# Performance work log

Hardware: AMD Instinct MI355X
Metric: run time of the kernel (lower is better)

The kernel has to match this reference:

```python
import jax, jax.numpy as jnp
import numpy as np

B, L, D, H, DEPTH, K = 16, 2048, 256, 8, 2, 7
HD = D // H
SCALE = HD ** -0.5


def _ln(x, g, b, eps=1e-5):
    m = x.mean(-1, keepdims=True)
    v = ((x - m) ** 2).mean(-1, keepdims=True)
    return (x - m) * jax.lax.rsqrt(v + eps) * g + b


def _nat_attn(x, qkv_w, qkv_b, proj_w, proj_b):
    # Neighborhood attention 1D: window of K tokens centered on each token,
    # clamped at sequence edges (NATTEN semantics, dilation=1).
    b, l, d = x.shape
    qkv = (x @ qkv_w + qkv_b).reshape(b, l, 3, H, HD).transpose(2, 0, 3, 1, 4)  # [3,B,H,L,hd]
    q, k, v = qkv[0] * SCALE, qkv[1], qkv[2]
    starts = jnp.clip(jnp.arange(l) - K // 2, 0, l - K)          # [L]
    idx = starts[:, None] + jnp.arange(K)                        # [L,K]
    kn = k[:, :, idx]                                            # [B,H,L,K,hd]
    vn = v[:, :, idx]
    attn = jax.nn.softmax(jnp.einsum('bhld,bhlkd->bhlk', q, kn), axis=-1)
    out = jnp.einsum('bhlk,bhlkd->bhld', attn, vn)               # [B,H,L,hd]
    out = out.transpose(0, 2, 1, 3).reshape(b, l, d)
    return out @ proj_w + proj_b


def _mlp(x, w1, b1, w2, b2):
    return jax.nn.gelu(x @ w1 + b1, approximate=False) @ w2 + b2


def setup_inputs() -> dict:
    key = jax.random.key(0)
    ks = jax.random.split(key, 8)
    s = 0.02
    return {
        'x': jax.random.normal(ks[0], (B, L, D), jnp.float32),
        'ln1_g': jnp.ones((DEPTH, D), jnp.float32),
        'ln1_b': jnp.zeros((DEPTH, D), jnp.float32),
        'qkv_w': jax.random.normal(ks[1], (DEPTH, D, 3 * D), jnp.float32) * s,
        'qkv_b': jnp.zeros((DEPTH, 3 * D), jnp.float32),
        'proj_w': jax.random.normal(ks[2], (DEPTH, D, D), jnp.float32) * s,
        'proj_b': jnp.zeros((DEPTH, D), jnp.float32),
        'ln2_g': jnp.ones((DEPTH, D), jnp.float32),
        'ln2_b': jnp.zeros((DEPTH, D), jnp.float32),
        'fc1_w': jax.random.normal(ks[3], (DEPTH, D, 4 * D), jnp.float32) * s,
        'fc1_b': jnp.zeros((DEPTH, 4 * D), jnp.float32),
        'fc2_w': jax.random.normal(ks[4], (DEPTH, 4 * D, D), jnp.float32) * s,
        'fc2_b': jnp.zeros((DEPTH, D), jnp.float32),
        'conv_w': jax.random.normal(ks[5], (2 * D, D, 3), jnp.float32) * s,  # OIH
        'dn_g': jnp.ones((2 * D,), jnp.float32),
        'dn_b': jnp.zeros((2 * D,), jnp.float32),
    }


def reference(x, ln1_g, ln1_b, qkv_w, qkv_b, proj_w, proj_b,
              ln2_g, ln2_b, fc1_w, fc1_b, fc2_w, fc2_b,
              conv_w, dn_g, dn_b):
    for i in range(DEPTH):
        h = _nat_attn(_ln(x, ln1_g[i], ln1_b[i]), qkv_w[i], qkv_b[i], proj_w[i], proj_b[i])
        x = x + h
        x = x + _mlp(_ln(x, ln2_g[i], ln2_b[i]), fc1_w[i], fc1_b[i], fc2_w[i], fc2_b[i])
    # ConvDownsampler: Conv1d(D, 2D, k=3, s=2, p=1, bias=False) + LayerNorm
    xc = x.transpose(0, 2, 1)  # [B,C,L]
    y = jax.lax.conv_general_dilated(xc, conv_w, window_strides=(2,),
                                     padding=[(1, 1)],
                                     dimension_numbers=('NCH', 'OIH', 'NCH'))
    y = y.transpose(0, 2, 1)   # [B, L//2, 2D]
    y = _ln(y, dn_g, dn_b)
    return (y, x)
```

## Files before the change

### kernel.cpp

```cpp
#include <hip/hip_runtime.h>

typedef unsigned short u16;
typedef __attribute__((ext_vector_type(8))) short bf16x8;
typedef __attribute__((ext_vector_type(4))) float f32x4;

__device__ __forceinline__ float bf2f(u16 u) { return __uint_as_float(((unsigned)u) << 16); }
__device__ __forceinline__ u16 f2bf(float f) {
    unsigned u = __float_as_uint(f);
    return (u16)((u + 0x7FFFu + ((u >> 16) & 1u)) >> 16);
}

__device__ __forceinline__ float gelu_fast(float v) {
    float u = v * (1.5957691216057308f + 0.07135481282700722f * v * v);
    return v * (1.f / (1.f + __expf(-u)));
}

__device__ __forceinline__ void load_lds16(const u16* g, u16* l) {
    __builtin_amdgcn_global_load_lds(
        (const __attribute__((address_space(1))) unsigned int*)g,
        (__attribute__((address_space(3))) unsigned int*)l,
        16, 0, 0);
}

template<int EPI>
__global__ __launch_bounds__(256) void gemm_kernel(
    const u16* __restrict__ A, const u16* __restrict__ Wt,
    const float* __restrict__ bias, const float* __restrict__ res,
    void* __restrict__ outp, int M, int N, int K)
{
    __shared__ __align__(16) u16 As[128 * 32];
    __shared__ __align__(16) u16 Bs[128 * 32];
    const int tid  = threadIdx.x;
    const int lane = tid & 63;
    const int wave = tid >> 6;
    const int row0 = blockIdx.x * 128;
    const int col0 = blockIdx.y * 128;
    const int wr = (wave >> 1) * 64;
    const int wc = (wave & 1) * 64;
    const int lr = lane & 15;
    const int kq = (lane >> 4) * 8;

    f32x4 acc[4][4];
#pragma unroll
    for (int i = 0; i < 4; ++i)
#pragma unroll
        for (int j = 0; j < 4; ++j) acc[i][j] = (f32x4){0.f, 0.f, 0.f, 0.f};

    const int srow = tid >> 2;
    const int scol = (tid & 3) * 8;
    const u16* ag = A  + (size_t)(row0 + srow) * K + scol;
    const u16* bg = Wt + (size_t)(col0 + srow) * K + scol;
    const size_t rstep = (size_t)64 * K;
    u16* alp = As + tid * 8;
    u16* blp = Bs + tid * 8;

    for (int k0 = 0; k0 < K; k0 += 32) {
        __syncthreads();
        load_lds16(ag + k0,         alp);
        load_lds16(ag + rstep + k0, alp + 64 * 32);
        load_lds16(bg + k0,         blp);
        load_lds16(bg + rstep + k0, blp + 64 * 32);
        __syncthreads();
        bf16x8 af[4], bfv[4];
#pragma unroll
        for (int i = 0; i < 4; ++i) af[i]  = *(const bf16x8*)(As + (wr + i * 16 + lr) * 32 + kq);
#pragma unroll
        for (int j = 0; j < 4; ++j) bfv[j] = *(const bf16x8*)(Bs + (wc + j * 16 + lr) * 32 + kq);
#pragma unroll
        for (int i = 0; i < 4; ++i)
#pragma unroll
            for (int j = 0; j < 4; ++j)
                acc[i][j] = __builtin_amdgcn_mfma_f32_16x16x32_bf16(af[i], bfv[j], acc[i][j], 0, 0, 0);
    }

#pragma unroll
    for (int i = 0; i < 4; ++i) {
        const int rbase = row0 + wr + i * 16 + (lane >> 4) * 4;
#pragma unroll
        for (int j = 0; j < 4; ++j) {
            const int col = col0 + wc + j * 16 + lr;
            const float bv = (EPI == 3) ? 0.f : bias[col];
#pragma unroll
            for (int r = 0; r < 4; ++r) {
                const int row = rbase + r;
                float v = acc[i][j][r] + bv;
                if (EPI == 1) {
                    v += res[(size_t)row * N + col];
                    ((float*)outp)[(size_t)row * N + col] = v;
                } else {
                    if (EPI == 2) v = gelu_fast(v);
                    ((u16*)outp)[(size_t)row * N + col] = f2bf(v);
                }
            }
        }
    }
}

__global__ __launch_bounds__(256) void ln_f2b_kernel(
    const float* __restrict__ x, const float* __restrict__ g,
    const float* __restrict__ be, u16* __restrict__ out)
{
    const int lane = threadIdx.x & 63;
    const int row  = blockIdx.x * 4 + (threadIdx.x >> 6);
    const float4 a = *(const float4*)(x + (size_t)row * 256 + lane * 4);
    float v[4] = {a.x, a.y, a.z, a.w};
    float s = v[0] + v[1] + v[2] + v[3];
#pragma unroll
    for (int m = 1; m < 64; m <<= 1) s += __shfl_xor(s, m);
    const float mean = s * (1.f / 256.f);
    float s2 = 0.f;
#pragma unroll
    for (int e = 0; e < 4; ++e) { float d = v[e] - mean; s2 += d * d; }
#pragma unroll
    for (int m = 1; m < 64; m <<= 1) s2 += __shfl_xor(s2, m);
    const float rstd = rsqrtf(s2 * (1.f / 256.f) + 1e-5f);
    const float4 gg = *(const float4*)(g + lane * 4);
    const float4 bb = *(const float4*)(be + lane * 4);
    ushort4 o;
    o.x = f2bf((v[0] - mean) * rstd * gg.x + bb.x);
    o.y = f2bf((v[1] - mean) * rstd * gg.y + bb.y);
    o.z = f2bf((v[2] - mean) * rstd * gg.z + bb.z);
    o.w = f2bf((v[3] - mean) * rstd * gg.w + bb.w);
    *(ushort4*)(out + (size_t)row * 256 + lane * 4) = o;
}

__global__ __launch_bounds__(256) void ln_b2f_kernel(
    const u16* __restrict__ x, const float* __restrict__ g,
    const float* __restrict__ be, float* __restrict__ out)
{
    const int lane = threadIdx.x & 63;
    const int row  = blockIdx.x * 4 + (threadIdx.x >> 6);
    const u16* xr = x + (size_t)row * 512 + lane * 8;
    float v[8];
#pragma unroll
    for (int e = 0; e < 8; e += 4) {
        ushort4 a = *(const ushort4*)(xr + e);
        v[e] = bf2f(a.x); v[e+1] = bf2f(a.y); v[e+2] = bf2f(a.z); v[e+3] = bf2f(a.w);
    }
    float s = 0.f;
#pragma unroll
    for (int e = 0; e < 8; ++e) s += v[e];
#pragma unroll
    for (int m = 1; m < 64; m <<= 1) s += __shfl_xor(s, m);
    const float mean = s * (1.f / 512.f);
    float s2 = 0.f;
#pragma unroll
    for (int e = 0; e < 8; ++e) { float d = v[e] - mean; s2 += d * d; }
#pragma unroll
    for (int m = 1; m < 64; m <<= 1) s2 += __shfl_xor(s2, m);
    const float rstd = rsqrtf(s2 * (1.f / 512.f) + 1e-5f);
    float* orow = out + (size_t)row * 512 + lane * 8;
#pragma unroll
    for (int e = 0; e < 8; e += 4) {
        float4 o;
        o.x = (v[e]   - mean) * rstd * g[lane*8+e]   + be[lane*8+e];
        o.y = (v[e+1] - mean) * rstd * g[lane*8+e+1] + be[lane*8+e+1];
        o.z = (v[e+2] - mean) * rstd * g[lane*8+e+2] + be[lane*8+e+2];
        o.w = (v[e+3] - mean) * rstd * g[lane*8+e+3] + be[lane*8+e+3];
        *(float4*)(orow + e) = o;
    }
}

__global__ __launch_bounds__(256) void attn_kernel(
    const u16* __restrict__ qkv, u16* __restrict__ out)
{
    const int lane  = threadIdx.x & 63;
    const int token = blockIdx.x * 4 + (threadIdx.x >> 6);
    const int b = token >> 11;
    const int l = token & 2047;
    const int h = lane >> 3;
    const int s = lane & 7;
    const int off = h * 32 + s * 4;

    ushort4 q4 = *(const ushort4*)(qkv + (size_t)token * 768 + off);
    const float scale = 0.17677669529663687f;
    float q0 = bf2f(q4.x), q1 = bf2f(q4.y), q2 = bf2f(q4.z), q3 = bf2f(q4.w);

    int start = l - 3;
    start = start < 0 ? 0 : (start > 2041 ? 2041 : start);
    const u16* kbase = qkv + ((size_t)(b << 11) + start) * 768 + 256 + off;

    float sc[7], vv[7][4];
#pragma unroll
    for (int j = 0; j < 7; ++j) {
        const u16* kp = kbase + (size_t)j * 768;
        ushort4 k4 = *(const ushort4*)kp;
        ushort4 v4 = *(const ushort4*)(kp + 256);
        float d = q0 * bf2f(k4.x) + q1 * bf2f(k4.y) + q2 * bf2f(k4.z) + q3 * bf2f(k4.w);
        d += __shfl_xor(d, 1); d += __shfl_xor(d, 2); d += __shfl_xor(d, 4);
        sc[j] = d * scale;
        vv[j][0] = bf2f(v4.x); vv[j][1] = bf2f(v4.y); vv[j][2] = bf2f(v4.z); vv[j][3] = bf2f(v4.w);
    }
    float mx = sc[0];
#pragma unroll
    for (int j = 1; j < 7; ++j) mx = fmaxf(mx, sc[j]);
    float p[7], sum = 0.f;
#pragma unroll
    for (int j = 0; j < 7; ++j) { p[j] = expf(sc[j] - mx); sum += p[j]; }
    const float inv = 1.f / sum;
    float o0 = 0, o1 = 0, o2 = 0, o3 = 0;
#pragma unroll
    for (int j = 0; j < 7; ++j) {
        o0 += p[j] * vv[j][0]; o1 += p[j] * vv[j][1];
        o2 += p[j] * vv[j][2]; o3 += p[j] * vv[j][3];
    }
    ushort4 o;
    o.x = f2bf(o0 * inv); o.y = f2bf(o1 * inv); o.z = f2bf(o2 * inv); o.w = f2bf(o3 * inv);
    *(ushort4*)(out + (size_t)token * 256 + off) = o;
}

__global__ void transpose_kernel(const float* __restrict__ in, u16* __restrict__ out,
                                 int K, int N, int total)
{
    int idx = blockIdx.x * 256 + threadIdx.x;
    if (idx >= total) return;
    int k = idx % K;
    int n = (idx / K) % N;
    int d = idx / (K * N);
    out[idx] = f2bf(in[(size_t)d * K * N + (size_t)k * N + n]);
}

__global__ void convw_kernel(const float* __restrict__ in, u16* __restrict__ out)
{
    int idx = blockIdx.x * 256 + threadIdx.x;
    int r  = idx % 768;
    int co = idx / 768;
    int t  = r / 256;
    int ci = r % 256;
    out[idx] = f2bf(in[(size_t)co * 768 + (size_t)ci * 3 + t]);
}

__global__ __launch_bounds__(256) void im2col_kernel(
    const float* __restrict__ x, u16* __restrict__ x2, int r0)
{
    int idx = blockIdx.x * 256 + threadIdx.x;
    int c4  = idx & 63;
    int t   = (idx >> 6) % 3;
    int rl  = idx / 192;
    int row = r0 + rl;
    int b   = row >> 10;
    int lo  = row & 1023;
    int l   = 2 * lo + t - 1;
    ushort4 o = {0, 0, 0, 0};
    if (l >= 0 && l < 2048) {
        float4 val = *(const float4*)(x + ((size_t)(b << 11) + l) * 256 + c4 * 4);
        o.x = f2bf(val.x); o.y = f2bf(val.y); o.z = f2bf(val.z); o.w = f2bf(val.w);
    }
    *(ushort4*)(x2 + (size_t)rl * 768 + t * 256 + c4 * 4) = o;
}

extern "C" void kernel_launch(void* const* d_in, const int* in_sizes, int n_in,
                              void* d_out, int out_size, void* d_ws, size_t ws_size,
                              hipStream_t stream)
{
    const float* x_in   = (const float*)d_in[0];
    const float* ln1_g  = (const float*)d_in[1];
    const float* ln1_b  = (const float*)d_in[2];
    const float* qkv_w  = (const float*)d_in[3];
    const float* qkv_b  = (const float*)d_in[4];
    const float* proj_w = (const float*)d_in[5];
    const float* proj_b = (const float*)d_in[6];
    const float* ln2_g  = (const float*)d_in[7];
    const float* ln2_b  = (const float*)d_in[8];
    const float* fc1_w  = (const float*)d_in[9];
    const float* fc1_b  = (const float*)d_in[10];
    const float* fc2_w  = (const float*)d_in[11];
    const float* fc2_b  = (const float*)d_in[12];
    const float* conv_w = (const float*)d_in[13];
    const float* dn_g   = (const float*)d_in[14];
    const float* dn_b   = (const float*)d_in[15];

    float* xbuf = (float*)d_out + 8388608;
    u16*   xn   = (u16*)d_out;

    char* ws = (char*)d_ws;
    const size_t MB = 1024ull * 1024;
    u16* qkv_wt  = (u16*)ws;
    u16* proj_wt = qkv_wt  + 2 * 768 * 256;
    u16* fc1_wt  = proj_wt + 2 * 256 * 256;
    u16* fc2_wt  = fc1_wt  + 2 * 1024 * 256;
    u16* conv_wt = fc2_wt  + 2 * 256 * 1024;
    u16* S       = (u16*)(ws + 4 * MB);

    const size_t R = ws_size > 4 * MB ? ws_size - 4 * MB : 0;
    int nb = 16;    while (nb > 1 && (size_t)nb * 4 * MB > R) nb >>= 1;
    int Mf = 32768; while (Mf > 2048 && (size_t)Mf * 2048 > R) Mf >>= 1;
    int Mc = 16384; while (Mc > 2048 && (size_t)Mc * 2560 > R) Mc >>= 1;

    transpose_kernel<<<(2*256*768 + 255) / 256, 256, 0, stream>>>(qkv_w,  qkv_wt,  256, 768, 2*256*768);
    transpose_kernel<<<(2*256*256 + 255) / 256, 256, 0, stream>>>(proj_w, proj_wt, 256, 256, 2*256*256);
    transpose_kernel<<<(2*256*1024 + 255) / 256, 256, 0, stream>>>(fc1_w, fc1_wt,  256, 1024, 2*256*1024);
    transpose_kernel<<<(2*1024*256 + 255) / 256, 256, 0, stream>>>(fc2_w, fc2_wt,  1024, 256, 2*1024*256);
    convw_kernel<<<(512*768) / 256, 256, 0, stream>>>(conv_w, conv_wt);

    hipMemcpyAsync(xbuf, x_in, 32768ull * 256 * 4, hipMemcpyDeviceToDevice, stream);

    for (int layer = 0; layer < 2; ++layer) {
        const float* l1g = ln1_g + layer * 256;
        const float* l1b = ln1_b + layer * 256;
        const float* l2g = ln2_g + layer * 256;
        const float* l2b = ln2_b + layer * 256;
        const u16*   qwt = qkv_wt  + (size_t)layer * 768 * 256;
        const float* qb  = qkv_b   + layer * 768;
        const u16*   pwt = proj_wt + (size_t)layer * 256 * 256;
        const float* pb  = proj_b  + layer * 256;
        const u16*   f1w = fc1_wt  + (size_t)layer * 1024 * 256;
        const float* f1b = fc1_b   + layer * 1024;
        const u16*   f2w = fc2_wt  + (size_t)layer * 256 * 1024;
        const float* f2b = fc2_b   + layer * 256;

        ln_f2b_kernel<<<8192, 256, 0, stream>>>(xbuf, l1g, l1b, xn);
        {
            const int Mg = nb * 2048;
            u16* qkvc  = S;
            u16* atnoc = S + (size_t)Mg * 768;
            for (int g = 0; g < 16 / nb; ++g) {
                const size_t t0 = (size_t)g * Mg;
                gemm_kernel<0><<<dim3(Mg / 128, 6), 256, 0, stream>>>(
                    xn + t0 * 256, qwt, qb, nullptr, qkvc, Mg, 768, 256);
                attn_kernel<<<Mg / 4, 256, 0, stream>>>(qkvc, atnoc);
                gemm_kernel<1><<<dim3(Mg / 128, 2), 256, 0, stream>>>(
                    atnoc, pwt, pb, xbuf + t0 * 256, xbuf + t0 * 256, Mg, 256, 256);
            }
        }
        ln_f2b_kernel<<<8192, 256, 0, stream>>>(xbuf, l2g, l2b, xn);
        {
            u16* hbuf = S;
            for (int q = 0; q < 32768 / Mf; ++q) {
                const size_t r0 = (size_t)q * Mf;
                gemm_kernel<2><<<dim3(Mf / 128, 8), 256, 0, stream>>>(
                    xn + r0 * 256, f1w, f1b, nullptr, hbuf, Mf, 1024, 256);
                gemm_kernel<1><<<dim3(Mf / 128, 2), 256, 0, stream>>>(
                    hbuf, f2w, f2b, xbuf + r0 * 256, xbuf + r0 * 256, Mf, 256, 1024);
            }
        }
    }

    {
        u16* x2c = S;
        u16* ycc = S + (size_t)Mc * 768;
        for (int c = 0; c < 16384 / Mc; ++c) {
            const int r0 = c * Mc;
            im2col_kernel<<<3 * Mc / 4, 256, 0, stream>>>(xbuf, x2c, r0);
            gemm_kernel<3><<<dim3(Mc / 128, 4), 256, 0, stream>>>(
                x2c, conv_wt, nullptr, nullptr, ycc, Mc, 512, 768);
            ln_b2f_kernel<<<Mc / 4, 256, 0, stream>>>(
                ycc, dn_g, dn_b, (float*)d_out + (size_t)r0 * 512);
        }
    }
}
```

Before: 525.4 us.

## Add K=256 GEMM kernel with LDS-resident weight panel and register-prefetched A

Adds a GEMM variant for K=256 that loads a full 128-column weight panel (pre-swizzled on device into an 8-wide K-chunk layout) into LDS once per block. Each block then walks several 128-row tiles, reading A fragments straight from global memory into registers with a three-deep prefetch instead of staging A in LDS with barriers. It is used for the QKV, proj and fc1 GEMMs, and the weights for those are repacked by a new swizzle kernel. The 64KB LDS per block limits occupancy, and the old gemm_kernel's GELU branch was removed (it now serves only fc2 and conv, which don't need GELU).

```diff
diff --git a/kernel.cpp b/kernel.cpp
--- a/kernel.cpp
+++ b/kernel.cpp
@@ -20,6 +20,89 @@
         (const __attribute__((address_space(1))) unsigned int*)g,
         (__attribute__((address_space(3))) unsigned int*)l,
         16, 0, 0);
+}
+
+template<int RT, int EPI>
+__global__ __launch_bounds__(256, 2) void gemm3_kernel(
+    const u16* __restrict__ A, const u16* __restrict__ Wsw,
+    const float* __restrict__ bias, const float* __restrict__ res,
+    void* __restrict__ outp, int M, int N)
+{
+    __shared__ __align__(16) u16 Bs[128 * 256];
+    const int tid  = threadIdx.x;
+    const int lane = tid & 63;
+    const int wave = tid >> 6;
+    const int pan  = blockIdx.y;
+    const int rowS = blockIdx.x * (RT * 128);
+    const int wr = (wave >> 1) * 64;
+    const int wc = (wave & 1) * 64;
+    const int lr = lane & 15;
+    const int kq = lane >> 4;
+
+    const u16* wsrc = Wsw + (size_t)pan * (256 * 128);
+#pragma unroll
+    for (int p = 0; p < 16; ++p)
+        load_lds16(wsrc + p * 2048 + tid * 8, Bs + p * 2048 + tid * 8);
+    __syncthreads();
+
+    const int col00 = pan * 128;
+    for (int rt = 0; rt < RT; ++rt) {
+        const int row0 = rowS + rt * 128;
+        const u16* arow = A + (size_t)(row0 + wr + lr) * 256 + kq * 8;
+
+        f32x4 acc[4][4];
+#pragma unroll
+        for (int i = 0; i < 4; ++i)
+#pragma unroll
+            for (int j = 0; j < 4; ++j) acc[i][j] = (f32x4){0.f, 0.f, 0.f, 0.f};
+
+        bf16x8 af[3][4];
+#pragma unroll
+        for (int i = 0; i < 4; ++i) af[0][i] = *(const bf16x8*)(arow + (size_t)i * 16 * 256);
+#pragma unroll
+        for (int i = 0; i < 4; ++i) af[1][i] = *(const bf16x8*)(arow + (size_t)i * 16 * 256 + 32);
+
+#pragma unroll
+        for (int kk = 0; kk < 8; ++kk) {
+            if (kk + 2 < 8) {
+                const int ko = (kk + 2) * 32;
+#pragma unroll
+                for (int i = 0; i < 4; ++i)
+                    af[(kk + 2) % 3][i] = *(const bf16x8*)(arow + (size_t)i * 16 * 256 + ko);
+            }
+            bf16x8 bfv[4];
+#pragma unroll
+            for (int j = 0; j < 4; ++j)
+                bfv[j] = *(const bf16x8*)(Bs + (size_t)((kk * 4 + kq) * 128 + wc + j * 16 + lr) * 8);
+#pragma unroll
+            for (int i = 0; i < 4; ++i)
+#pragma unroll
+                for (int j = 0; j < 4; ++j)
+                    acc[i][j] = __builtin_amdgcn_mfma_f32_16x16x32_bf16(af[kk % 3][i], bfv[j], acc[i][j], 0, 0, 0);
+        }
+
+#pragma unroll
+        for (int i = 0; i < 4; ++i) {
+            const int rbase = row0 + wr + i * 16 + (lane >> 4) * 4;
+#pragma unroll
+            for (int j = 0; j < 4; ++j) {
+                const int col = col00 + wc + j * 16 + lr;
+                const float bv = bias[col];
+#pragma unroll
+                for (int r = 0; r < 4; ++r) {
+                    const int row = rbase + r;
+                    float v = acc[i][j][r] + bv;
+                    if (EPI == 1) {
+                        v += res[(size_t)row * N + col];
+                        ((float*)outp)[(size_t)row * N + col] = v;
+                    } else {
+                        if (EPI == 2) v = gelu_fast(v);
+                        ((u16*)outp)[(size_t)row * N + col] = f2bf(v);
+                    }
+                }
+            }
+        }
+    }
 }
 
 template<int EPI>
@@ -88,12 +171,52 @@
                     v += res[(size_t)row * N + col];
                     ((float*)outp)[(size_t)row * N + col] = v;
                 } else {
-                    if (EPI == 2) v = gelu_fast(v);
                     ((u16*)outp)[(size_t)row * N + col] = f2bf(v);
                 }
             }
         }
     }
+}
+
+__global__ void wswz_kernel(const float* __restrict__ in, u16* __restrict__ out,
+                            int K, int N, int total)
+{
+    int g = blockIdx.x * 256 + threadIdx.x;
+    if (g >= total) return;
+    int nl  = g & 127;
+    int t   = g >> 7;
+    int kqq = t % (K >> 3);
+    int dp  = t / (K >> 3);
+    int p   = dp % (N >> 7);
+    int d   = dp / (N >> 7);
+    int n_g = p * 128 + nl;
+    int k0  = kqq * 8;
+    const float* s = in + ((size_t)d * K + k0) * N + n_g;
+    u16 o[8];
+#pragma unroll
+    for (int e = 0; e < 8; ++e) o[e] = f2bf(s[(size_t)e * N]);
+    *(uint4*)(out + (size_t)g * 8) = *(const uint4*)o;
+}
+
+__global__ void transpose_kernel(const float* __restrict__ in, u16* __restrict__ out,
+                                 int K, int N, int total)
+{
+    int idx = blockIdx.x * 256 + threadIdx.x;
+    if (idx >= total) return;
+    int k = idx % K;
+    int n = (idx / K) % N;
+    int d = idx / (K * N);
+    out[idx] = f2bf(in[(size_t)d * K * N + (size_t)k * N + n]);
+}
+
+__global__ void convw_kernel(const float* __restrict__ in, u16* __restrict__ out)
+{
+    int idx = blockIdx.x * 256 + threadIdx.x;
+    int r  = idx % 768;
+    int co = idx / 768;
+    int t  = r / 256;
+    int ci = r % 256;
+    out[idx] = f2bf(in[(size_t)co * 768 + (size_t)ci * 3 + t]);
 }
 
 __global__ __launch_bounds__(256) void ln_f2b_kernel(
@@ -207,27 +330,6 @@
     ushort4 o;
     o.x = f2bf(o0 * inv); o.y = f2bf(o1 * inv); o.z = f2bf(o2 * inv); o.w = f2bf(o3 * inv);
     *(ushort4*)(out + (size_t)token * 256 + off) = o;
-}
-
-__global__ void transpose_kernel(const float* __restrict__ in, u16* __restrict__ out,
-                                 int K, int N, int total)
-{
-    int idx = blockIdx.x * 256 + threadIdx.x;
-    if (idx >= total) return;
-    int k = idx % K;
-    int n = (idx / K) % N;
-    int d = idx / (K * N);
-    out[idx] = f2bf(in[(size_t)d * K * N + (size_t)k * N + n]);
-}
-
-__global__ void convw_kernel(const float* __restrict__ in, u16* __restrict__ out)
-{
-    int idx = blockIdx.x * 256 + threadIdx.x;
-    int r  = idx % 768;
-    int co = idx / 768;
-    int t  = r / 256;
-    int ci = r % 256;
-    out[idx] = f2bf(in[(size_t)co * 768 + (size_t)ci * 3 + t]);
 }
 
 __global__ __launch_bounds__(256) void im2col_kernel(
@@ -287,10 +389,10 @@
     int Mf = 32768; while (Mf > 2048 && (size_t)Mf * 2048 > R) Mf >>= 1;
     int Mc = 16384; while (Mc > 2048 && (size_t)Mc * 2560 > R) Mc >>= 1;
 
-    transpose_kernel<<<(2*256*768 + 255) / 256, 256, 0, stream>>>(qkv_w,  qkv_wt,  256, 768, 2*256*768);
-    transpose_kernel<<<(2*256*256 + 255) / 256, 256, 0, stream>>>(proj_w, proj_wt, 256, 256, 2*256*256);
-    transpose_kernel<<<(2*256*1024 + 255) / 256, 256, 0, stream>>>(fc1_w, fc1_wt,  256, 1024, 2*256*1024);
-    transpose_kernel<<<(2*1024*256 + 255) / 256, 256, 0, stream>>>(fc2_w, fc2_wt,  1024, 256, 2*1024*256);
+    wswz_kernel<<<(2*256*768/8 + 255) / 256, 256, 0, stream>>>(qkv_w,  qkv_wt,  256, 768,  2*256*768/8);
+    wswz_kernel<<<(2*256*256/8 + 255) / 256, 256, 0, stream>>>(proj_w, proj_wt, 256, 256,  2*256*256/8);
+    wswz_kernel<<<(2*256*1024/8 + 255) / 256, 256, 0, stream>>>(fc1_w, fc1_wt,  256, 1024, 2*256*1024/8);
+    transpose_kernel<<<(2*1024*256 + 255) / 256, 256, 0, stream>>>(fc2_w, fc2_wt, 1024, 256, 2*1024*256);
     convw_kernel<<<(512*768) / 256, 256, 0, stream>>>(conv_w, conv_wt);
 
     hipMemcpyAsync(xbuf, x_in, 32768ull * 256 * 4, hipMemcpyDeviceToDevice, stream);
@@ -316,11 +418,11 @@
             u16* atnoc = S + (size_t)Mg * 768;
             for (int g = 0; g < 16 / nb; ++g) {
                 const size_t t0 = (size_t)g * Mg;
-                gemm_kernel<0><<<dim3(Mg / 128, 6), 256, 0, stream>>>(
-                    xn + t0 * 256, qwt, qb, nullptr, qkvc, Mg, 768, 256);
+                gemm3_kernel<4, 0><<<dim3(Mg / 512, 6), 256, 0, stream>>>(
+                    xn + t0 * 256, qwt, qb, nullptr, qkvc, Mg, 768);
                 attn_kernel<<<Mg / 4, 256, 0, stream>>>(qkvc, atnoc);
-                gemm_kernel<1><<<dim3(Mg / 128, 2), 256, 0, stream>>>(
-                    atnoc, pwt, pb, xbuf + t0 * 256, xbuf + t0 * 256, Mg, 256, 256);
+                gemm3_kernel<2, 1><<<dim3(Mg / 256, 2), 256, 0, stream>>>(
+                    atnoc, pwt, pb, xbuf + t0 * 256, xbuf + t0 * 256, Mg, 256);
             }
         }
         ln_f2b_kernel<<<8192, 256, 0, stream>>>(xbuf, l2g, l2b, xn);
@@ -328,8 +430,8 @@
             u16* hbuf = S;
             for (int q = 0; q < 32768 / Mf; ++q) {
                 const size_t r0 = (size_t)q * Mf;
-                gemm_kernel<2><<<dim3(Mf / 128, 8), 256, 0, stream>>>(
-                    xn + r0 * 256, f1w, f1b, nullptr, hbuf, Mf, 1024, 256);
+                gemm3_kernel<4, 2><<<dim3(Mf / 512, 8), 256, 0, stream>>>(
+                    xn + r0 * 256, f1w, f1b, nullptr, hbuf, Mf, 1024);
                 gemm_kernel<1><<<dim3(Mf / 128, 2), 256, 0, stream>>>(
                     hbuf, f2w, f2b, xbuf + r0 * 256, xbuf + r0 * 256, Mf, 256, 1024);
             }
```

Result: slower. 545.3 us (+3.8%).

## Double GEMM K-tile to 64 and XOR-swizzle LDS layout to avoid bank conflicts

Applied to the files above, without the earlier changes.

The GEMM main loop now stages a 128x64 K-slice per iteration instead of 128x32, which halves the number of barrier pairs per K. Each thread's global-to-LDS chunk index is XOR-swizzled by its row, and fragment reads apply the same swizzle so LDS reads hit fewer bank conflicts. LDS use per block doubles to 32 KB, which may reduce occupancy, and K must be a multiple of 64.

```diff
diff --git a/kernel.cpp b/kernel.cpp
--- a/kernel.cpp
+++ b/kernel.cpp
@@ -28,8 +28,8 @@
     const float* __restrict__ bias, const float* __restrict__ res,
     void* __restrict__ outp, int M, int N, int K)
 {
-    __shared__ __align__(16) u16 As[128 * 32];
-    __shared__ __align__(16) u16 Bs[128 * 32];
+    __shared__ __align__(16) u16 As[128 * 64];
+    __shared__ __align__(16) u16 Bs[128 * 64];
     const int tid  = threadIdx.x;
     const int lane = tid & 63;
     const int wave = tid >> 6;
@@ -38,7 +38,7 @@
     const int wr = (wave >> 1) * 64;
     const int wc = (wave & 1) * 64;
     const int lr = lane & 15;
-    const int kq = (lane >> 4) * 8;
+    const int q  = lane >> 4;
 
     f32x4 acc[4][4];
 #pragma unroll
@@ -46,31 +46,41 @@
 #pragma unroll
         for (int j = 0; j < 4; ++j) acc[i][j] = (f32x4){0.f, 0.f, 0.f, 0.f};
 
-    const int srow = tid >> 2;
-    const int scol = (tid & 3) * 8;
-    const u16* ag = A  + (size_t)(row0 + srow) * K + scol;
-    const u16* bg = Wt + (size_t)(col0 + srow) * K + scol;
-    const size_t rstep = (size_t)64 * K;
+    const int strow  = tid >> 3;
+    const int schunk = (tid & 7) ^ (strow & 7);
+    const u16* ag = A  + (size_t)(row0 + strow) * K + schunk * 8;
+    const u16* bg = Wt + (size_t)(col0 + strow) * K + schunk * 8;
+    const size_t rstep32 = (size_t)32 * K;
     u16* alp = As + tid * 8;
     u16* blp = Bs + tid * 8;
 
-    for (int k0 = 0; k0 < K; k0 += 32) {
+    for (int k0 = 0; k0 < K; k0 += 64) {
         __syncthreads();
-        load_lds16(ag + k0,         alp);
-        load_lds16(ag + rstep + k0, alp + 64 * 32);
-        load_lds16(bg + k0,         blp);
-        load_lds16(bg + rstep + k0, blp + 64 * 32);
+#pragma unroll
+        for (int s = 0; s < 4; ++s) {
+            load_lds16(ag + s * rstep32 + k0, alp + s * 2048);
+            load_lds16(bg + s * rstep32 + k0, blp + s * 2048);
+        }
         __syncthreads();
-        bf16x8 af[4], bfv[4];
-#pragma unroll
-        for (int i = 0; i < 4; ++i) af[i]  = *(const bf16x8*)(As + (wr + i * 16 + lr) * 32 + kq);
-#pragma unroll
-        for (int j = 0; j < 4; ++j) bfv[j] = *(const bf16x8*)(Bs + (wc + j * 16 + lr) * 32 + kq);
-#pragma unroll
-        for (int i = 0; i < 4; ++i)
-#pragma unroll
-            for (int j = 0; j < 4; ++j)
-                acc[i][j] = __builtin_amdgcn_mfma_f32_16x16x32_bf16(af[i], bfv[j], acc[i][j], 0, 0, 0);
+#pragma unroll
+        for (int kk = 0; kk < 2; ++kk) {
+            bf16x8 af[4], bfv[4];
+#pragma unroll
+            for (int i = 0; i < 4; ++i) {
+                const int r = wr + i * 16 + lr;
+                af[i] = *(const bf16x8*)(As + r * 64 + (((kk * 4 + q) ^ (r & 7)) * 8));
+            }
+#pragma unroll
+            for (int j = 0; j < 4; ++j) {
+                const int r = wc + j * 16 + lr;
+                bfv[j] = *(const bf16x8*)(Bs + r * 64 + (((kk * 4 + q) ^ (r & 7)) * 8));
+            }
+#pragma unroll
+            for (int i = 0; i < 4; ++i)
+#pragma unroll
+                for (int j = 0; j < 4; ++j)
+                    acc[i][j] = __builtin_amdgcn_mfma_f32_16x16x32_bf16(af[i], bfv[j], acc[i][j], 0, 0, 0);
+        }
     }
 
 #pragma unroll
```

Measured after the change: 501.0 us. 1.05x faster.
